# Kernel optimization log

Measured on AMD Instinct MI355X. Metric: run time of the kernel, lower is better.

The kernel has to match this reference:

```python
import jax, jax.numpy as jnp
import numpy as np

# Static architecture of the decoded CNN (matches init_kwargs index_dict)
KERNEL_NO = [64, 128, 256]
KERNEL_SIZE = [9, 9, 9]
CH_IN = [3, 64, 128]
IDX_START = [0, 1792, 75648]
I_DIM = 370816  # last slice's last index + 1
D_MODEL = 512
BATCH = 128
N_LAYERS = len(KERNEL_NO)


def _build_slices():
    """Replicates DebedderNeuron.get_kernel_slices(); per-layer int32 index matrix [K_l, L_l]."""
    sl = []
    for idx in range(N_LAYERS):
        rows = []
        for kd in range(KERNEL_NO[idx]):
            s = IDX_START[idx] + kd * KERNEL_SIZE[idx] * CH_IN[idx]
            e = s + KERNEL_SIZE[idx] * CH_IN[idx]
            bias = IDX_START[idx] + KERNEL_NO[idx] * KERNEL_SIZE[idx] * CH_IN[idx] + kd
            ik = list(range(s, e)) + [bias]
            if idx < N_LAYERS - 1:
                for kn in range(KERNEL_NO[idx + 1]):
                    ns = (IDX_START[idx + 1] + kd * KERNEL_SIZE[idx + 1]
                          + kn * CH_IN[idx + 1] * KERNEL_SIZE[idx + 1])
                    ik.extend(range(ns, ns + KERNEL_SIZE[idx + 1]))
            rows.append(ik)
        sl.append(jnp.asarray(np.array(rows, dtype=np.int32)))
    return sl

IDX = _build_slices()  # lengths per row: [1180, 2881, 1153]


def setup_inputs() -> dict:
    key = jax.random.key(0)
    ks = jax.random.split(key, 7)
    dims = [int(IDX[l].shape[1]) for l in range(N_LAYERS)]
    inp = {"x": jax.random.normal(ks[0], (BATCH, sum(KERNEL_NO), D_MODEL), jnp.float32)}
    for l in range(N_LAYERS):
        inp[f"W{l}"] = jax.random.normal(ks[1 + 2 * l], (D_MODEL, dims[l]), jnp.float32) * 0.02
        inp[f"b{l}"] = jax.random.normal(ks[2 + 2 * l], (dims[l],), jnp.float32) * 0.02
    return inp


def reference(x, W0, b0, W1, b1, W2, b2):
    # One shared Linear per CNN layer (as in the torch module); batch all kernels of a
    # layer into a single GEMM, then scatter-add into the flat weight vector y.
    Ws = [W0, W1, W2]
    bs = [b0, b1, b2]
    y = jnp.zeros((x.shape[0], I_DIM), x.dtype)
    off = 0
    for l in range(N_LAYERS):
        K = KERNEL_NO[l]
        yt = jnp.einsum('bkd,di->bki', x[:, off:off + K], Ws[l]) + bs[l]  # [B, K_l, L_l]
        y = y.at[:, IDX[l]].add(yt)  # overlapping scatter-add, matches sequential += in torch
        off += K
    # middle layers are written twice (own slice + previous layer's extension) -> halve
    y = y.at[:, IDX_START[1]:IDX_START[-1]].multiply(0.5)
    return y
```

## Files before the change

### kernel.cpp

```cpp
#include <hip/hip_runtime.h>
#include <cstdint>

typedef short short8 __attribute__((ext_vector_type(8)));
typedef float f32x4 __attribute__((ext_vector_type(4)));

#define LDS_AS3(p) ((__attribute__((address_space(3))) unsigned*)(p))
#define GLB_AS1(p) ((const __attribute__((address_space(1))) unsigned*)(p))

__device__ inline unsigned bfpack(float a, float b) {
    union { float f; unsigned u; } ua, ub;
    ua.f = a; ub.f = b;
    unsigned lo = (ua.u + 0x7FFFu + ((ua.u >> 16) & 1u)) >> 16;
    unsigned hi = (ub.u + 0x7FFFu + ((ub.u >> 16) & 1u)) & 0xFFFF0000u;
    return lo | hi;
}
__device__ inline unsigned short bf16of(float a) { return (unsigned short)bfpack(a, 0.0f); }
__device__ inline float bf2f(unsigned short s) {
    union { unsigned u; float f; } x; x.u = (unsigned)s << 16; return x.f;
}

__global__ __launch_bounds__(256)
void cvt_x(const float* __restrict__ X, unsigned short* __restrict__ XB)
{
    const int g = blockIdx.x * 256 + threadIdx.x;
    const float4 v0 = *(const float4*)(X + (size_t)g * 8);
    const float4 v1 = *(const float4*)(X + (size_t)g * 8 + 4);
    uint4 u;
    u.x = bfpack(v0.x, v0.y); u.y = bfpack(v0.z, v0.w);
    u.z = bfpack(v1.x, v1.y); u.w = bfpack(v1.z, v1.w);
    *(uint4*)(XB + (size_t)g * 8) = u;
}

template <int N>
__global__ __launch_bounds__(256)
void cvt_w(const float* __restrict__ W, unsigned short* __restrict__ WT)
{
    const int g = blockIdx.x * 256 + threadIdx.x;
    if (g >= N * 64) return;
    const int n = g % N, d8 = g / N;
    const float* p = W + (size_t)d8 * 8 * N + n;
    uint4 u;
    u.x = bfpack(p[0],             p[(size_t)N]);
    u.y = bfpack(p[2 * (size_t)N], p[3 * (size_t)N]);
    u.z = bfpack(p[4 * (size_t)N], p[5 * (size_t)N]);
    u.w = bfpack(p[6 * (size_t)N], p[7 * (size_t)N]);
    *(uint4*)(WT + (size_t)n * 512 + d8 * 8) = u;
}

template <int MODE>
__global__ __launch_bounds__(1024, 4)
void gemm_big(const unsigned short* __restrict__ XB,
              const unsigned short* __restrict__ WT,
              const float* __restrict__ BIAS, float* __restrict__ Y,
              const unsigned short* __restrict__ EXTI,
              unsigned short* __restrict__ EXTO)
{
    constexpr int K_L  = (MODE == 0) ? 64 : (MODE == 1) ? 128 : 256;
    constexpr int LOGK = (MODE == 0) ? 6  : (MODE == 1) ? 7   : 8;
    constexpr int N    = (MODE == 0) ? 1180 : (MODE == 1) ? 2881 : 1153;
    constexpr int XOFF = (MODE == 0) ? 0 : (MODE == 1) ? 64 : 192;
    constexpr int NT   = (N + 255) / 256;

    __shared__ __align__(16) unsigned short lA[2][256 * 64];
    __shared__ __align__(16) unsigned short lB[2][256 * 64];

    const int t    = threadIdx.x;
    const int lane = t & 63;
    const int wv   = t >> 6;
    const int wr   = wv >> 2;
    const int wc   = wv & 3;
    const int kq   = lane >> 4;
    const int lr16 = lane & 15;

    const int cpx = (int)gridDim.x >> 3;
    const int wg  = (blockIdx.x & 7) * cpx + (blockIdx.x >> 3);
    const int nt  = wg % NT;
    const int mt  = wg / NT;
    const int m0  = mt * 256;
    const int n0  = nt * 256;

    auto stage = [&](int buf, int kt) {
        #pragma unroll
        for (int i = 0; i < 2; ++i) {
            const int c   = i * 1024 + t;
            const int row = c >> 3, p = c & 7, l = p ^ (row & 7);
            const int m   = m0 + row;
            const int b   = m >> LOGK, kd = m & (K_L - 1);
            const unsigned short* gp =
                XB + ((size_t)(b * 448 + XOFF + kd) << 9) + kt * 64 + l * 8;
            __builtin_amdgcn_global_load_lds(GLB_AS1(gp),
                LDS_AS3(&lA[buf][c * 8]), 16, 0, 0);
        }
        #pragma unroll
        for (int i = 0; i < 2; ++i) {
            const int c   = i * 1024 + t;
            const int row = c >> 3, p = c & 7, l = p ^ (row & 7);
            int gc = n0 + row; if (gc > N - 1) gc = N - 1;
            const unsigned short* gp = WT + (size_t)gc * 512 + kt * 64 + l * 8;
            __builtin_amdgcn_global_load_lds(GLB_AS1(gp),
                LDS_AS3(&lB[buf][c * 8]), 16, 0, 0);
        }
    };

    f32x4 acc[4][4] = {};

    stage(0, 0);
    __syncthreads();

    #pragma unroll 1
    for (int kt = 0; kt < 8; ++kt) {
        const int buf = kt & 1;
        if (kt < 7) stage(buf ^ 1, kt + 1);

        #pragma unroll
        for (int ks = 0; ks < 2; ++ks) {
            const int s = ks * 4 + kq;
            short8 af[4], bf[4];
            #pragma unroll
            for (int mi = 0; mi < 4; ++mi) {
                const int row = wr * 64 + mi * 16 + lr16;
                af[mi] = *(const short8*)(&lA[buf][row * 64 + ((s ^ (row & 7)) * 8)]);
            }
            #pragma unroll
            for (int ni = 0; ni < 4; ++ni) {
                const int row = wc * 64 + ni * 16 + lr16;
                bf[ni] = *(const short8*)(&lB[buf][row * 64 + ((s ^ (row & 7)) * 8)]);
            }
            __builtin_amdgcn_s_setprio(1);
            #pragma unroll
            for (int mi = 0; mi < 4; ++mi)
                #pragma unroll
                for (int ni = 0; ni < 4; ++ni)
                    acc[mi][ni] = __builtin_amdgcn_mfma_f32_16x16x32_bf16(
                        af[mi], bf[ni], acc[mi][ni], 0, 0, 0);
            __builtin_amdgcn_s_setprio(0);
        }
        __syncthreads();
    }

    #pragma unroll
    for (int ni = 0; ni < 4; ++ni) {
        const int n = n0 + wc * 64 + ni * 16 + lr16;
        if (n >= N) continue;
        const float bias = BIAS[n];
        #pragma unroll
        for (int mi = 0; mi < 4; ++mi) {
            #pragma unroll
            for (int r = 0; r < 4; ++r) {
                const int m  = m0 + wr * 64 + mi * 16 + kq * 4 + r;
                const int b  = m >> LOGK;
                const int kd = m & (K_L - 1);
                const float v = acc[mi][ni][r] + bias;
                float* yb = Y + (size_t)b * 370816;
                if constexpr (MODE == 0) {
                    if (n < 27)       yb[kd * 27 + n] = v;
                    else if (n == 27) yb[1728 + kd]   = v;
                    else EXTO[((size_t)(b * 64 + kd)) * 1152 + (n - 28)] = bf16of(v);
                } else if constexpr (MODE == 1) {
                    if (n < 576) {
                        const float e = bf2f(EXTI[((size_t)(b * 64 + n / 9)) * 1152 + kd * 9 + n % 9]);
                        yb[1792 + kd * 576 + n] = 0.5f * (v + e);
                    } else if (n == 576) yb[75520 + kd] = 0.5f * v;
                    else EXTO[((size_t)(b * 128 + kd)) * 2304 + (n - 577)] = bf16of(v);
                } else {
                    if (n < 1152) {
                        const float e = bf2f(EXTI[((size_t)(b * 128 + n / 9)) * 2304 + kd * 9 + n % 9]);
                        yb[75648 + kd * 1152 + n] = v + e;
                    } else yb[370560 + kd] = v;
                }
            }
        }
    }
}

extern "C" void kernel_launch(void* const* d_in, const int* in_sizes, int n_in,
                              void* d_out, int out_size, void* d_ws, size_t ws_size,
                              hipStream_t stream)
{
    const float* x  = (const float*)d_in[0];
    const float* W0 = (const float*)d_in[1];
    const float* b0 = (const float*)d_in[2];
    const float* W1 = (const float*)d_in[3];
    const float* b1 = (const float*)d_in[4];
    const float* W2 = (const float*)d_in[5];
    const float* b2 = (const float*)d_in[6];
    float* y = (float*)d_out;

    unsigned short* XB   = (unsigned short*)d_ws;
    unsigned short* WT0  = XB   + (size_t)128 * 448 * 512;
    unsigned short* WT1  = WT0  + (size_t)1180 * 512;
    unsigned short* WT2  = WT1  + (size_t)2881 * 512;
    unsigned short* EXT0 = WT2  + (size_t)1153 * 512;
    unsigned short* EXT1 = EXT0 + (size_t)128 * 64 * 1152;

    cvt_x<<<dim3(14336), 256, 0, stream>>>(x, XB);
    cvt_w<1180><<<dim3((1180 * 64 + 255) / 256), 256, 0, stream>>>(W0, WT0);
    cvt_w<2881><<<dim3((2881 * 64 + 255) / 256), 256, 0, stream>>>(W1, WT1);
    cvt_w<1153><<<dim3((1153 * 64 + 255) / 256), 256, 0, stream>>>(W2, WT2);

    gemm_big<0><<<dim3(32 * 5),   1024, 0, stream>>>(XB, WT0, b0, y, nullptr, EXT0);
    gemm_big<1><<<dim3(64 * 12),  1024, 0, stream>>>(XB, WT1, b1, y, EXT0, EXT1);
    gemm_big<2><<<dim3(128 * 5),  1024, 0, stream>>>(XB, WT2, b2, y, EXT1, nullptr);
}
```

Measured before the change: 308.2 us.

## Stage GEMM epilogue through LDS for coalesced vectorized stores and extension reads

The epilogue now writes the accumulators into an LDS tile and has each wave emit full rows with float4/uint2 stores, instead of scattered per-element stores. Tiles are classified so interior tiles take a vector fast path. Layer 2 loads its bf16 extension panel into LDS with a padded stride (E1S=2308, stored shifted by one) to avoid strided gathers from global memory. This adds extra LDS passes and syncs in the epilogue and an enlarged shared buffer, which may limit occupancy.

```diff
diff --git a/kernel.cpp b/kernel.cpp
--- a/kernel.cpp
+++ b/kernel.cpp
@@ -18,6 +18,8 @@
 __device__ inline float bf2f(unsigned short s) {
     union { unsigned u; float f; } x; x.u = (unsigned)s << 16; return x.f;
 }
+
+constexpr int E1S = 2308;
 
 __global__ __launch_bounds__(256)
 void cvt_x(const float* __restrict__ X, unsigned short* __restrict__ XB)
@@ -61,8 +63,9 @@
     constexpr int XOFF = (MODE == 0) ? 0 : (MODE == 1) ? 64 : 192;
     constexpr int NT   = (N + 255) / 256;
 
-    __shared__ __align__(16) unsigned short lA[2][256 * 64];
-    __shared__ __align__(16) unsigned short lB[2][256 * 64];
+    __shared__ __align__(16) char smem[133120];
+    unsigned short* lAp = (unsigned short*)smem;
+    unsigned short* lBp = lAp + 2 * 256 * 64;
 
     const int t    = threadIdx.x;
     const int lane = t & 63;
@@ -89,7 +92,7 @@
             const unsigned short* gp =
                 XB + ((size_t)(b * 448 + XOFF + kd) << 9) + kt * 64 + l * 8;
             __builtin_amdgcn_global_load_lds(GLB_AS1(gp),
-                LDS_AS3(&lA[buf][c * 8]), 16, 0, 0);
+                LDS_AS3(lAp + buf * 16384 + c * 8), 16, 0, 0);
         }
         #pragma unroll
         for (int i = 0; i < 2; ++i) {
@@ -98,7 +101,7 @@
             int gc = n0 + row; if (gc > N - 1) gc = N - 1;
             const unsigned short* gp = WT + (size_t)gc * 512 + kt * 64 + l * 8;
             __builtin_amdgcn_global_load_lds(GLB_AS1(gp),
-                LDS_AS3(&lB[buf][c * 8]), 16, 0, 0);
+                LDS_AS3(lBp + buf * 16384 + c * 8), 16, 0, 0);
         }
     };
 
@@ -106,12 +109,10 @@
 
     stage(0, 0);
     __syncthreads();
-
     #pragma unroll 1
     for (int kt = 0; kt < 8; ++kt) {
         const int buf = kt & 1;
         if (kt < 7) stage(buf ^ 1, kt + 1);
-
         #pragma unroll
         for (int ks = 0; ks < 2; ++ks) {
             const int s = ks * 4 + kq;
@@ -119,12 +120,12 @@
             #pragma unroll
             for (int mi = 0; mi < 4; ++mi) {
                 const int row = wr * 64 + mi * 16 + lr16;
-                af[mi] = *(const short8*)(&lA[buf][row * 64 + ((s ^ (row & 7)) * 8)]);
+                af[mi] = *(const short8*)(lAp + buf * 16384 + row * 64 + ((s ^ (row & 7)) * 8));
             }
             #pragma unroll
             for (int ni = 0; ni < 4; ++ni) {
                 const int row = wc * 64 + ni * 16 + lr16;
-                bf[ni] = *(const short8*)(&lB[buf][row * 64 + ((s ^ (row & 7)) * 8)]);
+                bf[ni] = *(const short8*)(lBp + buf * 16384 + row * 64 + ((s ^ (row & 7)) * 8));
             }
             __builtin_amdgcn_s_setprio(1);
             #pragma unroll
@@ -138,35 +139,113 @@
         __syncthreads();
     }
 
-    #pragma unroll
-    for (int ni = 0; ni < 4; ++ni) {
-        const int n = n0 + wc * 64 + ni * 16 + lr16;
-        if (n >= N) continue;
-        const float bias = BIAS[n];
-        #pragma unroll
-        for (int mi = 0; mi < 4; ++mi) {
-            #pragma unroll
-            for (int r = 0; r < 4; ++r) {
-                const int m  = m0 + wr * 64 + mi * 16 + kq * 4 + r;
-                const int b  = m >> LOGK;
-                const int kd = m & (K_L - 1);
-                const float v = acc[mi][ni][r] + bias;
-                float* yb = Y + (size_t)b * 370816;
-                if constexpr (MODE == 0) {
-                    if (n < 27)       yb[kd * 27 + n] = v;
-                    else if (n == 27) yb[1728 + kd]   = v;
-                    else EXTO[((size_t)(b * 64 + kd)) * 1152 + (n - 28)] = bf16of(v);
-                } else if constexpr (MODE == 1) {
-                    if (n < 576) {
-                        const float e = bf2f(EXTI[((size_t)(b * 64 + n / 9)) * 1152 + kd * 9 + n % 9]);
-                        yb[1792 + kd * 576 + n] = 0.5f * (v + e);
-                    } else if (n == 576) yb[75520 + kd] = 0.5f * v;
-                    else EXTO[((size_t)(b * 128 + kd)) * 2304 + (n - 577)] = bf16of(v);
+    constexpr int RPP   = (MODE == 2) ? 64 : 128;
+    constexpr int NPASS = 256 / RPP;
+    constexpr int RPW   = RPP / 16;
+    float* LDSf = (float*)smem;
+    unsigned short* panel = (unsigned short*)(smem + 66560);
+
+    const int cls = (MODE == 0) ? ((n0 == 0 || n0 + 255 >= N) ? 2 : 1)
+                  : (MODE == 1) ? ((n0 + 255 < 576) ? 0 : (n0 <= 576) ? 2
+                                   : (n0 + 255 < N) ? 1 : 2)
+                  :               ((n0 + 255 < 1152) ? 0 : 2);
+
+    #pragma unroll 1
+    for (int h = 0; h < NPASS; ++h) {
+        if (h) __syncthreads();
+        const bool mine = (MODE == 2) ? (wr == h) : ((wr >> 1) == h);
+        if (mine) {
+            const int mb = (MODE == 2) ? 0 : (wr & 1) * 64;
+            #pragma unroll
+            for (int mi = 0; mi < 4; ++mi)
+                #pragma unroll
+                for (int ni = 0; ni < 4; ++ni)
+                    #pragma unroll
+                    for (int r = 0; r < 4; ++r)
+                        LDSf[(mb + mi * 16 + kq * 4 + r) * 260 + wc * 64 + ni * 16 + lr16]
+                            = acc[mi][ni][r];
+        }
+        int row_lo = 0;
+        if constexpr (MODE == 2) {
+            row_lo = n0 / 9;
+            const int ntop  = (n0 + 256 <= 1152) ? (n0 + 255) : 1151;
+            const int nrows = ntop / 9 - row_lo + 1;
+            const int col0  = h * 576;
+            const int bB    = m0 >> 8;
+            for (int t2 = t; t2 < nrows * 145; t2 += 1024) {
+                const int rr2 = t2 / 145, cc = t2 % 145;
+                const uint2 v = *(const uint2*)(EXTI +
+                    ((size_t)(bB * 128 + row_lo + rr2)) * E1S + col0 + cc * 4);
+                *(uint2*)(panel + rr2 * 584 + cc * 4) = v;
+            }
+        }
+        __syncthreads();
+
+        #pragma unroll 1
+        for (int rr = 0; rr < RPW; ++rr) {
+            const int ml = wv * RPW + rr;
+            const int m  = m0 + h * RPP + ml;
+            const int b  = m >> LOGK;
+            const int kd = m & (K_L - 1);
+            const int nb = n0 + lane * 4;
+            const float4 v4 = *(const float4*)&LDSf[ml * 260 + lane * 4];
+            float* yb = Y + (size_t)b * 370816;
+
+            if (cls == 0) {
+                const float4 b4 = *(const float4*)(BIAS + nb);
+                float e[4];
+                if constexpr (MODE == 1) {
+                    #pragma unroll
+                    for (int i = 0; i < 4; ++i) {
+                        const int n = nb + i;
+                        e[i] = bf2f(EXTI[((size_t)(b * 64 + n / 9)) * 1152 + kd * 9 + n % 9]);
+                    }
+                    float4 o;
+                    o.x = 0.5f * (v4.x + b4.x + e[0]); o.y = 0.5f * (v4.y + b4.y + e[1]);
+                    o.z = 0.5f * (v4.z + b4.z + e[2]); o.w = 0.5f * (v4.w + b4.w + e[3]);
+                    *(float4*)(yb + 1792 + kd * 576 + nb) = o;
                 } else {
-                    if (n < 1152) {
-                        const float e = bf2f(EXTI[((size_t)(b * 128 + n / 9)) * 2304 + kd * 9 + n % 9]);
-                        yb[75648 + kd * 1152 + n] = v + e;
-                    } else yb[370560 + kd] = v;
+                    #pragma unroll
+                    for (int i = 0; i < 4; ++i) {
+                        const int n = nb + i;
+                        e[i] = bf2f(panel[(n / 9 - row_lo) * 584 + ml * 9 + n % 9 + 1]);
+                    }
+                    float4 o;
+                    o.x = v4.x + b4.x + e[0]; o.y = v4.y + b4.y + e[1];
+                    o.z = v4.z + b4.z + e[2]; o.w = v4.w + b4.w + e[3];
+                    *(float4*)(yb + 75648 + kd * 1152 + nb) = o;
+                }
+            } else if (cls == 1) {
+                const float4 b4 = *(const float4*)(BIAS + nb);
+                uint2 u;
+                u.x = bfpack(v4.x + b4.x, v4.y + b4.y);
+                u.y = bfpack(v4.z + b4.z, v4.w + b4.w);
+                if constexpr (MODE == 0)
+                    *(uint2*)(EXTO + ((size_t)(b * 64 + kd)) * 1152 + (nb - 28)) = u;
+                else
+                    *(uint2*)(EXTO + ((size_t)(b * 128 + kd)) * E1S + (nb - 576)) = u;
+            } else {
+                #pragma unroll
+                for (int i = 0; i < 4; ++i) {
+                    const int n = nb + i;
+                    if (n >= N) continue;
+                    const float v = ((const float*)&v4)[i] + BIAS[n];
+                    if constexpr (MODE == 0) {
+                        if (n < 27)       yb[kd * 27 + n] = v;
+                        else if (n == 27) yb[1728 + kd]   = v;
+                        else EXTO[((size_t)(b * 64 + kd)) * 1152 + (n - 28)] = bf16of(v);
+                    } else if constexpr (MODE == 1) {
+                        if (n < 576) {
+                            const float e = bf2f(EXTI[((size_t)(b * 64 + n / 9)) * 1152 + kd * 9 + n % 9]);
+                            yb[1792 + kd * 576 + n] = 0.5f * (v + e);
+                        } else if (n == 576) yb[75520 + kd] = 0.5f * v;
+                        else EXTO[((size_t)(b * 128 + kd)) * E1S + (n - 576)] = bf16of(v);
+                    } else {
+                        if (n < 1152) {
+                            const float e = bf2f(panel[(n / 9 - row_lo) * 584 + ml * 9 + n % 9 + 1]);
+                            yb[75648 + kd * 1152 + n] = v + e;
+                        } else if (n == 1152) yb[370560 + kd] = v;
+                    }
                 }
             }
         }
@@ -198,7 +277,7 @@
     cvt_w<2881><<<dim3((2881 * 64 + 255) / 256), 256, 0, stream>>>(W1, WT1);
     cvt_w<1153><<<dim3((1153 * 64 + 255) / 256), 256, 0, stream>>>(W2, WT2);
 
-    gemm_big<0><<<dim3(32 * 5),   1024, 0, stream>>>(XB, WT0, b0, y, nullptr, EXT0);
-    gemm_big<1><<<dim3(64 * 12),  1024, 0, stream>>>(XB, WT1, b1, y, EXT0, EXT1);
-    gemm_big<2><<<dim3(128 * 5),  1024, 0, stream>>>(XB, WT2, b2, y, EXT1, nullptr);
-}
+    gemm_big<0><<<dim3(32 * 5),  1024, 0, stream>>>(XB, WT0, b0, y, nullptr, EXT0);
+    gemm_big<1><<<dim3(64 * 12), 1024, 0, stream>>>(XB, WT1, b1, y, EXT0, EXT1);
+    gemm_big<2><<<dim3(128 * 5), 1024, 0, stream>>>(XB, WT2, b2, y, EXT1, nullptr);
+}
```

Result: faster. 293.9 us (-4.7%).

## Stage GEMM epilogue through LDS and transpose extension buffers for coalesced access

Applied to the files above, without the earlier changes.

The epilogue now spills accumulators into a padded LDS tile, in two halves, and writes outputs row-wise, using float4 stores where possible. The intermediate extension buffers are stored transposed, so the next layer reads them contiguously (uint2 loads) rather than with strided gathers through n/9 and n%9. The aim is to replace scattered global reads and writes in the epilogue with coalesced ones. In exchange it adds extra syncs, a larger shared-memory allocation that may reduce occupancy, and more intricate index logic.

```diff
diff --git a/kernel.cpp b/kernel.cpp
--- a/kernel.cpp
+++ b/kernel.cpp
@@ -15,9 +15,7 @@
     return lo | hi;
 }
 __device__ inline unsigned short bf16of(float a) { return (unsigned short)bfpack(a, 0.0f); }
-__device__ inline float bf2f(unsigned short s) {
-    union { unsigned u; float f; } x; x.u = (unsigned)s << 16; return x.f;
-}
+__device__ inline float ubits(unsigned u) { union { unsigned x; float f; } c; c.x = u; return c.f; }
 
 __global__ __launch_bounds__(256)
 void cvt_x(const float* __restrict__ X, unsigned short* __restrict__ XB)
@@ -61,8 +59,9 @@
     constexpr int XOFF = (MODE == 0) ? 0 : (MODE == 1) ? 64 : 192;
     constexpr int NT   = (N + 255) / 256;
 
-    __shared__ __align__(16) unsigned short lA[2][256 * 64];
-    __shared__ __align__(16) unsigned short lB[2][256 * 64];
+    __shared__ __align__(16) char smem[133120];
+    unsigned short* lAp = (unsigned short*)smem;
+    unsigned short* lBp = lAp + 2 * 256 * 64;
 
     const int t    = threadIdx.x;
     const int lane = t & 63;
@@ -89,7 +88,7 @@
             const unsigned short* gp =
                 XB + ((size_t)(b * 448 + XOFF + kd) << 9) + kt * 64 + l * 8;
             __builtin_amdgcn_global_load_lds(GLB_AS1(gp),
-                LDS_AS3(&lA[buf][c * 8]), 16, 0, 0);
+                LDS_AS3(lAp + buf * 16384 + c * 8), 16, 0, 0);
         }
         #pragma unroll
         for (int i = 0; i < 2; ++i) {
@@ -98,7 +97,7 @@
             int gc = n0 + row; if (gc > N - 1) gc = N - 1;
             const unsigned short* gp = WT + (size_t)gc * 512 + kt * 64 + l * 8;
             __builtin_amdgcn_global_load_lds(GLB_AS1(gp),
-                LDS_AS3(&lB[buf][c * 8]), 16, 0, 0);
+                LDS_AS3(lBp + buf * 16384 + c * 8), 16, 0, 0);
         }
     };
 
@@ -106,12 +105,10 @@
 
     stage(0, 0);
     __syncthreads();
-
     #pragma unroll 1
     for (int kt = 0; kt < 8; ++kt) {
         const int buf = kt & 1;
         if (kt < 7) stage(buf ^ 1, kt + 1);
-
         #pragma unroll
         for (int ks = 0; ks < 2; ++ks) {
             const int s = ks * 4 + kq;
@@ -119,12 +116,12 @@
             #pragma unroll
             for (int mi = 0; mi < 4; ++mi) {
                 const int row = wr * 64 + mi * 16 + lr16;
-                af[mi] = *(const short8*)(&lA[buf][row * 64 + ((s ^ (row & 7)) * 8)]);
+                af[mi] = *(const short8*)(lAp + buf * 16384 + row * 64 + ((s ^ (row & 7)) * 8));
             }
             #pragma unroll
             for (int ni = 0; ni < 4; ++ni) {
                 const int row = wc * 64 + ni * 16 + lr16;
-                bf[ni] = *(const short8*)(&lB[buf][row * 64 + ((s ^ (row & 7)) * 8)]);
+                bf[ni] = *(const short8*)(lBp + buf * 16384 + row * 64 + ((s ^ (row & 7)) * 8));
             }
             __builtin_amdgcn_s_setprio(1);
             #pragma unroll
@@ -138,36 +135,129 @@
         __syncthreads();
     }
 
-    #pragma unroll
-    for (int ni = 0; ni < 4; ++ni) {
-        const int n = n0 + wc * 64 + ni * 16 + lr16;
-        if (n >= N) continue;
-        const float bias = BIAS[n];
-        #pragma unroll
-        for (int mi = 0; mi < 4; ++mi) {
-            #pragma unroll
-            for (int r = 0; r < 4; ++r) {
-                const int m  = m0 + wr * 64 + mi * 16 + kq * 4 + r;
-                const int b  = m >> LOGK;
-                const int kd = m & (K_L - 1);
-                const float v = acc[mi][ni][r] + bias;
-                float* yb = Y + (size_t)b * 370816;
-                if constexpr (MODE == 0) {
-                    if (n < 27)       yb[kd * 27 + n] = v;
-                    else if (n == 27) yb[1728 + kd]   = v;
-                    else EXTO[((size_t)(b * 64 + kd)) * 1152 + (n - 28)] = bf16of(v);
-                } else if constexpr (MODE == 1) {
+    float* LDSf = (float*)smem;
+
+    #pragma unroll 1
+    for (int h = 0; h < 2; ++h) {
+        if (h) __syncthreads();
+        if ((wr >> 1) == h) {
+            const int mb = (wr & 1) * 64;
+            #pragma unroll
+            for (int mi = 0; mi < 4; ++mi)
+                #pragma unroll
+                for (int ni = 0; ni < 4; ++ni)
+                    #pragma unroll
+                    for (int r = 0; r < 4; ++r)
+                        LDSf[(mb + mi * 16 + kq * 4 + r) * 260 + wc * 64 + ni * 16 + lr16]
+                            = acc[mi][ni][r];
+        }
+        __syncthreads();
+
+        if constexpr (MODE == 0) {
+            const int lo = (n0 > 28) ? n0 : 28;
+            const int hi = (n0 + 256 < 1180) ? n0 + 256 : 1180;
+            const int kn_lo = (lo - 28) / 9, kn_hi = (hi - 29) / 9;
+            const int b_base = (m0 + h * 128) >> 6;
+            #pragma unroll 1
+            for (int idx = wv; idx < 2 * (kn_hi - kn_lo + 1); idx += 16) {
+                const int bloc = idx & 1, kn = kn_lo + (idx >> 1);
+                unsigned short* dst = EXTO + ((size_t)((b_base + bloc) * 128 + kn)) * 576;
+                #pragma unroll
+                for (int i = 0; i < 9; ++i) {
+                    const int col = i * 64 + lane;
+                    const int kd0 = col / 9, j = col - kd0 * 9;
+                    const int n = 28 + kn * 9 + j;
+                    if (n >= lo && n < hi)
+                        dst[col] = bf16of(LDSf[(bloc * 64 + kd0) * 260 + (n - n0)] + BIAS[n]);
+                }
+            }
+            if (n0 == 0) {
+                #pragma unroll 1
+                for (int rr = 0; rr < 8; ++rr) {
+                    const int ml = wv * 8 + rr;
+                    const int m  = m0 + h * 128 + ml;
+                    const int b  = m >> 6, kd = m & 63;
+                    float* yb = Y + (size_t)b * 370816;
+                    if (lane < 27)       yb[kd * 27 + lane] = LDSf[ml * 260 + lane] + BIAS[lane];
+                    else if (lane == 27) yb[1728 + kd]      = LDSf[ml * 260 + 27] + BIAS[27];
+                }
+            }
+        } else if constexpr (MODE == 1) {
+            const int lo = (n0 > 577) ? n0 : 577;
+            const int hi = (n0 + 256 < 2881) ? n0 + 256 : 2881;
+            const int b  = (m0 >> 7) + h;
+            if (lo < hi) {
+                const int k_lo = (lo - 577) / 9, k_hi = (hi - 578) / 9;
+                #pragma unroll 1
+                for (int idx = wv; idx <= k_hi - k_lo; idx += 16) {
+                    const int kn2 = k_lo + idx;
+                    unsigned short* dst = EXTO + ((size_t)(b * 256 + kn2)) * 1152;
+                    #pragma unroll
+                    for (int i = 0; i < 18; ++i) {
+                        const int col = i * 64 + lane;
+                        const int kd1 = col / 9, j = col - kd1 * 9;
+                        const int n = 577 + kn2 * 9 + j;
+                        if (n >= lo && n < hi)
+                            dst[col] = bf16of(LDSf[kd1 * 260 + (n - n0)] + BIAS[n]);
+                    }
+                }
+            }
+            if (n0 + 255 < 576) {
+                #pragma unroll 1
+                for (int rr = 0; rr < 8; ++rr) {
+                    const int ml = wv * 8 + rr;
+                    const int m  = m0 + h * 128 + ml;
+                    const int bb = m >> 7, kd = m & 127;
+                    const int nb = n0 + lane * 4;
+                    const float4 v4 = *(const float4*)&LDSf[ml * 260 + lane * 4];
+                    const float4 b4 = *(const float4*)(BIAS + nb);
+                    const uint2 e2 = *(const uint2*)(EXTI + ((size_t)(bb * 128 + kd)) * 576 + nb);
+                    float4 o;
+                    o.x = 0.5f * (v4.x + b4.x + ubits(e2.x << 16));
+                    o.y = 0.5f * (v4.y + b4.y + ubits(e2.x & 0xFFFF0000u));
+                    o.z = 0.5f * (v4.z + b4.z + ubits(e2.y << 16));
+                    o.w = 0.5f * (v4.w + b4.w + ubits(e2.y & 0xFFFF0000u));
+                    *(float4*)(Y + (size_t)bb * 370816 + 1792 + kd * 576 + nb) = o;
+                }
+            } else if (n0 <= 576) {
+                #pragma unroll 1
+                for (int rr = 0; rr < 8; ++rr) {
+                    const int ml = wv * 8 + rr;
+                    const int m  = m0 + h * 128 + ml;
+                    const int bb = m >> 7, kd = m & 127;
+                    const int n  = n0 + lane;
                     if (n < 576) {
-                        const float e = bf2f(EXTI[((size_t)(b * 64 + n / 9)) * 1152 + kd * 9 + n % 9]);
-                        yb[1792 + kd * 576 + n] = 0.5f * (v + e);
-                    } else if (n == 576) yb[75520 + kd] = 0.5f * v;
-                    else EXTO[((size_t)(b * 128 + kd)) * 2304 + (n - 577)] = bf16of(v);
-                } else {
-                    if (n < 1152) {
-                        const float e = bf2f(EXTI[((size_t)(b * 128 + n / 9)) * 2304 + kd * 9 + n % 9]);
-                        yb[75648 + kd * 1152 + n] = v + e;
-                    } else yb[370560 + kd] = v;
-                }
+                        const float e = ubits((unsigned)EXTI[((size_t)(bb * 128 + kd)) * 576 + n] << 16);
+                        Y[(size_t)bb * 370816 + 1792 + kd * 576 + n] =
+                            0.5f * (LDSf[ml * 260 + lane] + BIAS[n] + e);
+                    }
+                    if (lane == 0)
+                        Y[(size_t)bb * 370816 + 75520 + kd] =
+                            0.5f * (LDSf[ml * 260 + 64] + BIAS[576]);
+                }
+            }
+        } else {
+            const int hi_own = (n0 + 256 < 1152) ? n0 + 256 : 1152;
+            #pragma unroll 1
+            for (int rr = 0; rr < 8; ++rr) {
+                const int ml = wv * 8 + rr;
+                const int m  = m0 + h * 128 + ml;
+                const int bb = m >> 8, kd = m & 255;
+                const int nb = n0 + lane * 4;
+                float* yb = Y + (size_t)bb * 370816;
+                if (nb + 3 < hi_own) {
+                    const float4 v4 = *(const float4*)&LDSf[ml * 260 + lane * 4];
+                    const float4 b4 = *(const float4*)(BIAS + nb);
+                    const uint2 e2 = *(const uint2*)(EXTI + ((size_t)(bb * 256 + kd)) * 1152 + nb);
+                    float4 o;
+                    o.x = v4.x + b4.x + ubits(e2.x << 16);
+                    o.y = v4.y + b4.y + ubits(e2.x & 0xFFFF0000u);
+                    o.z = v4.z + b4.z + ubits(e2.y << 16);
+                    o.w = v4.w + b4.w + ubits(e2.y & 0xFFFF0000u);
+                    *(float4*)(yb + 75648 + kd * 1152 + nb) = o;
+                }
+                if (n0 + 256 > 1152 && lane == 32)
+                    yb[370560 + kd] = LDSf[ml * 260 + 128] + BIAS[1152];
             }
         }
     }
@@ -186,19 +276,19 @@
     const float* b2 = (const float*)d_in[6];
     float* y = (float*)d_out;
 
-    unsigned short* XB   = (unsigned short*)d_ws;
-    unsigned short* WT0  = XB   + (size_t)128 * 448 * 512;
-    unsigned short* WT1  = WT0  + (size_t)1180 * 512;
-    unsigned short* WT2  = WT1  + (size_t)2881 * 512;
-    unsigned short* EXT0 = WT2  + (size_t)1153 * 512;
-    unsigned short* EXT1 = EXT0 + (size_t)128 * 64 * 1152;
+    unsigned short* XB    = (unsigned short*)d_ws;
+    unsigned short* WT0   = XB    + (size_t)128 * 448 * 512;
+    unsigned short* WT1   = WT0   + (size_t)1180 * 512;
+    unsigned short* WT2   = WT1   + (size_t)2881 * 512;
+    unsigned short* EXT0T = WT2   + (size_t)1153 * 512;
+    unsigned short* EXT1T = EXT0T + (size_t)128 * 128 * 576;
 
     cvt_x<<<dim3(14336), 256, 0, stream>>>(x, XB);
     cvt_w<1180><<<dim3((1180 * 64 + 255) / 256), 256, 0, stream>>>(W0, WT0);
     cvt_w<2881><<<dim3((2881 * 64 + 255) / 256), 256, 0, stream>>>(W1, WT1);
     cvt_w<1153><<<dim3((1153 * 64 + 255) / 256), 256, 0, stream>>>(W2, WT2);
 
-    gemm_big<0><<<dim3(32 * 5),   1024, 0, stream>>>(XB, WT0, b0, y, nullptr, EXT0);
-    gemm_big<1><<<dim3(64 * 12),  1024, 0, stream>>>(XB, WT1, b1, y, EXT0, EXT1);
-    gemm_big<2><<<dim3(128 * 5),  1024, 0, stream>>>(XB, WT2, b2, y, EXT1, nullptr);
-}
+    gemm_big<0><<<dim3(32 * 5),  1024, 0, stream>>>(XB, WT0, b0, y, nullptr, EXT0T);
+    gemm_big<1><<<dim3(64 * 12), 1024, 0, stream>>>(XB, WT1, b1, y, EXT0T, EXT1T);
+    gemm_big<2><<<dim3(128 * 5), 1024, 0, stream>>>(XB, WT2, b2, y, EXT1T, nullptr);
+}
```

After: 426.8 us. 1.38x slower.
